# Kernel tuning notes

Measured on AMD Instinct MI355X. Metric: run time of the kernel, lower is better.

Reference implementation:

```python
import jax, jax.numpy as jnp
import numpy as np

L, D, K, NUM_CLASSES, HID = 512, 128, 1, 3, 128
EPS = 1e-8


def setup_inputs() -> dict:
    key = jax.random.key(0)
    ks = jax.random.split(key, 8)
    B, N = 16, 16384
    x = jax.random.normal(ks[0], (B, N, L), dtype=jnp.float32)
    mask = jnp.ones((B, N), dtype=jnp.float32)
    # params stored as [in, out] (equivalent to torch Linear with W.T)
    Wv = jax.random.normal(ks[1], (L, D), dtype=jnp.float32) * (1.0 / np.sqrt(L))
    bv = jnp.zeros((D,), dtype=jnp.float32)
    Wu = jax.random.normal(ks[2], (L, D), dtype=jnp.float32) * (1.0 / np.sqrt(L))
    bu = jnp.zeros((D,), dtype=jnp.float32)
    Wa = jax.random.normal(ks[3], (D, K), dtype=jnp.float32) * (1.0 / np.sqrt(D))
    ba = jnp.zeros((K,), dtype=jnp.float32)
    W1 = jax.random.normal(ks[4], (L, HID), dtype=jnp.float32) * (1.0 / np.sqrt(L))
    b1 = jnp.zeros((HID,), dtype=jnp.float32)
    W2 = jax.random.normal(ks[5], (HID, NUM_CLASSES), dtype=jnp.float32) * (1.0 / np.sqrt(HID))
    b2 = jnp.zeros((NUM_CLASSES,), dtype=jnp.float32)
    return {"x": x, "mask": mask, "Wv": Wv, "bv": bv, "Wu": Wu, "bu": bu,
            "Wa": Wa, "ba": ba, "W1": W1, "b1": b1, "W2": W2, "b2": b2,
            "top_k": 70}


def reference(x, mask, Wv, bv, Wu, bu, Wa, ba, W1, b1, W2, b2, top_k):
    # gated attention scores: [B, N]
    A_V = jnp.tanh(jnp.einsum('bnl,ld->bnd', x, Wv) + bv)
    A_U = jax.nn.sigmoid(jnp.einsum('bnl,ld->bnd', x, Wu) + bu)
    A = jnp.einsum('bnd,dk->bnk', A_V * A_U, Wa) + ba   # [B, N, K=1]
    A = jax.nn.softmax(A, axis=1)[..., 0]               # [B, N]
    # mask + renormalize
    A = A * mask
    A = A / (jnp.sum(A, axis=1, keepdims=True) + EPS)
    # dropout is identity in eval mode
    k = min(top_k, x.shape[1])
    topk_vals, topk_idxs = jax.lax.top_k(A, k)          # [B, k]
    # gather full feature vectors of top-k patches, mean pool
    topk_features = jnp.take_along_axis(x, topk_idxs[..., None], axis=1)  # [B, k, L]
    pooled = jnp.mean(topk_features, axis=1)            # [B, L]
    # classifier MLP
    h = jax.nn.relu(pooled @ W1 + b1)
    Y_prob = h @ W2 + b2                                # [B, num_classes]
    Y_hat = jnp.argmax(Y_prob, axis=1)
    return Y_prob, Y_hat, A
```

## Files before the change

### kernel.cpp

```cpp
#include <hip/hip_runtime.h>
#include <math.h>

#define NB   16
#define NN   16384
#define LDIM 512
#define DDIM 128
#define HIDD 128
#define NCLS 3
#define KCAP 256
#define CCAP 1024
#define ROWB 8
#define EPSV 1e-8f
#define DELTA 0.02f

typedef float  f32x4  __attribute__((ext_vector_type(4)));
typedef int    i32x4  __attribute__((ext_vector_type(4)));
typedef unsigned u32x2 __attribute__((ext_vector_type(2)));
typedef __bf16 bf16x8 __attribute__((ext_vector_type(8)));
typedef unsigned long long u64;

__device__ __forceinline__ int get_k(const int* kp) {
    int k = kp[0];
    if (k < 1 || k > NN) {
        float f = __int_as_float(k);
        if (f >= 1.0f && f <= (float)NN) k = (int)f;
        else k = 70;
    }
    if (k > NN) k = NN;
    return k;
}

__device__ __forceinline__ unsigned okey(float f) {
    unsigned u = __float_as_uint(f);
    return (u & 0x80000000u) ? ~u : (u | 0x80000000u);
}
__device__ __forceinline__ float inv_okey(unsigned k) {
    unsigned u = (k & 0x80000000u) ? (k & 0x7FFFFFFFu) : ~k;
    return __uint_as_float(u);
}

__device__ __forceinline__ unsigned pk2bf(float a, float b) {
    unsigned ua = __float_as_uint(a); ua = (ua + 0x7FFFu + ((ua >> 16) & 1u)) >> 16;
    unsigned ub = __float_as_uint(b); ub = (ub + 0x7FFFu + ((ub >> 16) & 1u)) & 0xFFFF0000u;
    return (ua & 0xFFFFu) | ub;
}

__device__ __forceinline__ f32x4 mfma16(i32x4 a, i32x4 b, f32x4 c) {
    return __builtin_amdgcn_mfma_f32_16x16x32_bf16(
        __builtin_bit_cast(bf16x8, a), __builtin_bit_cast(bf16x8, b), c, 0, 0, 0);
}

__device__ __forceinline__ float sig_fast(float v)  { return 1.0f / (1.0f + __expf(-v)); }
__device__ __forceinline__ float tanh_fast(float v) { return 1.0f - 2.0f / (1.0f + __expf(2.0f * v)); }

__global__ void k0_prep(const float* __restrict__ Wv, const float* __restrict__ Wu,
                        unsigned short* __restrict__ Wp)
{
    int i = blockIdx.x * 256 + threadIdx.x;
    int g   = i >> 16;
    int rem = i & 65535;
    int kd  = rem >> 7;
    int n   = rem & 127;
    float w = g ? Wu[rem] : Wv[rem];
    unsigned u = __float_as_uint(w);
    u = (u + 0x7FFFu + ((u >> 16) & 1u)) >> 16;
    int kt = kd >> 5, lg = (kd >> 3) & 3, j = kd & 7, nt = n >> 4, lr = n & 15;
    Wp[kt * 8192 + g * 4096 + nt * 512 + lg * 128 + lr * 8 + j] = (unsigned short)u;
}

__global__ __launch_bounds__(512, 1)
void k1_mfma(const float* __restrict__ x, const unsigned short* __restrict__ Wp,
             const float* __restrict__ bv, const float* __restrict__ bu,
             const float* __restrict__ Wa, const float* __restrict__ ba,
             float* __restrict__ logits)
{
    __shared__ __align__(16) char lds[98304];

    const int t   = threadIdx.x;
    const int wid = t >> 6;
    const int l   = t & 63;
    const int lr  = l & 15;
    const int lg  = l >> 4;
    const int l7  = lr & 7;

    i32x4 Wreg[2][16];
    {
        const unsigned short* wb = Wp + wid * 512 + l * 8;
#pragma unroll
        for (int kt = 0; kt < 16; ++kt) {
#pragma unroll
            for (int g = 0; g < 2; ++g)
                Wreg[g][kt] = *(const i32x4*)(wb + kt * 8192 + g * 4096);
        }
    }

    const int dbase = wid * 16 + lg * 4;
    float bvR[4], buR[4], waR[4];
#pragma unroll
    for (int r = 0; r < 4; ++r) {
        bvR[r] = bv[dbase + r]; buR[r] = bu[dbase + r]; waR[r] = Wa[dbase + r];
    }
    const float ba0 = ba[0];

    const int c     = t & 127;
    const int r0    = t >> 7;
    const int chalf = c & 1;
    const int clog  = c >> 1;

    const size_t blk_row0 = (size_t)blockIdx.x * 1024;
    const float* xblk = x + blk_row0 * LDIM;
    float* sEp = (float*)(lds + 65536);

    f32x4 acc[2][2];
    f32x4 xg[8];

#pragma unroll
    for (int i = 0; i < 8; ++i)
        xg[i] = *(const f32x4*)(xblk + (size_t)(i * 4 + r0) * LDIM + c * 4);
#pragma unroll
    for (int i = 0; i < 8; ++i) {
        int row = i * 4 + r0;
        u32x2 wv; wv.x = pk2bf(xg[i].x, xg[i].y); wv.y = pk2bf(xg[i].z, xg[i].w);
        *(u32x2*)(lds + row * 1024 + ((clog ^ (row & 7)) * 16) + chalf * 8) = wv;
    }
    __syncthreads();

    int p = 0;
    for (int j = 0; j < 32; ++j) {
        const bool has_next = (j < 31);
        if (has_next) {
            const float* xt = xblk + (size_t)(j + 1) * 32 * LDIM;
#pragma unroll
            for (int i = 0; i < 8; ++i)
                xg[i] = *(const f32x4*)(xt + (size_t)(i * 4 + r0) * LDIM + c * 4);
        }
#pragma unroll
        for (int g = 0; g < 2; ++g)
#pragma unroll
            for (int rf = 0; rf < 2; ++rf)
                acc[g][rf] = f32x4{0.f, 0.f, 0.f, 0.f};
        const char* Xb = lds + p * 32768;
#pragma unroll
        for (int kt = 0; kt < 16; ++kt) {
            i32x4 b0 = *(const i32x4*)(Xb + lr * 1024        + (((kt * 4 + lg) ^ l7) * 16));
            i32x4 b1 = *(const i32x4*)(Xb + (16 + lr) * 1024 + (((kt * 4 + lg) ^ l7) * 16));
            acc[0][0] = mfma16(Wreg[0][kt], b0, acc[0][0]);
            acc[1][0] = mfma16(Wreg[1][kt], b0, acc[1][0]);
            acc[0][1] = mfma16(Wreg[0][kt], b1, acc[0][1]);
            acc[1][1] = mfma16(Wreg[1][kt], b1, acc[1][1]);
        }
        if (has_next) {
            char* Xw = lds + (p ^ 1) * 32768;
#pragma unroll
            for (int i = 0; i < 8; ++i) {
                int row = i * 4 + r0;
                u32x2 wv; wv.x = pk2bf(xg[i].x, xg[i].y); wv.y = pk2bf(xg[i].z, xg[i].w);
                *(u32x2*)(Xw + row * 1024 + ((clog ^ (row & 7)) * 16) + chalf * 8) = wv;
            }
        }
#pragma unroll
        for (int rf = 0; rf < 2; ++rf) {
            float s = 0.f;
#pragma unroll
            for (int r = 0; r < 4; ++r) {
                float vv = tanh_fast(acc[0][rf][r] + bvR[r]);
                float uu = sig_fast (acc[1][rf][r] + buR[r]);
                s = fmaf(vv * uu, waR[r], s);
            }
            s += __shfl_xor(s, 16);
            s += __shfl_xor(s, 32);
            if (l < 16) sEp[wid * 1024 + j * 32 + rf * 16 + l] = s;
        }
        __syncthreads();
        p ^= 1;
    }

#pragma unroll
    for (int rr = 0; rr < 2; ++rr) {
        int row = t + rr * 512;
        float s = ba0;
#pragma unroll
        for (int w2 = 0; w2 < 8; ++w2) s += sEp[w2 * 1024 + row];
        logits[blk_row0 + row] = s;
    }
}

__global__ __launch_bounds__(1024, 1)
void k3a_band_softmax(float* __restrict__ A, const float* __restrict__ mask,
                      const int* __restrict__ kp, int* __restrict__ idxWS,
                      int* __restrict__ candIdx, int* __restrict__ counts)
{
    __shared__ float sredf[16];
    __shared__ int   sredi[2][16];
    __shared__ int sIn, sCand;
    const int b = blockIdx.x;
    const int t = threadIdx.x;
    const int w = t >> 6;
    int k = get_k(kp); if (k > KCAP) k = KCAP;
    float* Ab = A + (size_t)b * NN;
    const float* mb = mask + (size_t)b * NN;

    float raw[16]; unsigned mbits = 0u;
#pragma unroll
    for (int j = 0; j < 16; ++j) {
        int i = t + j * 1024;
        raw[j] = Ab[i];
        if (mb[i] > 0.0f) mbits |= (1u << j);
    }
    unsigned kk[16];
#pragma unroll
    for (int j = 0; j < 16; ++j) {
        float v = ((mbits >> j) & 1) ? raw[j] : -3.0e38f;
        kk[j] = okey(v);
    }
    unsigned lo = 0u, hi = 0xFFFFFFFFu;
    int par = 0;
    while (lo < hi) {
        unsigned span = hi - lo;
        unsigned mid = lo + (span >> 1) + (span & 1u);
        int c = 0;
#pragma unroll
        for (int j = 0; j < 16; ++j) c += (kk[j] >= mid) ? 1 : 0;
#pragma unroll
        for (int m2 = 1; m2 < 64; m2 <<= 1) c += __shfl_xor(c, m2);
        if ((t & 63) == 0) sredi[par][w] = c;
        __syncthreads();
        c = 0;
#pragma unroll
        for (int w2 = 0; w2 < 16; ++w2) c += sredi[par][w2];
        if (c >= k) lo = mid; else hi = mid - 1;
        par ^= 1;
    }
    const float tv = inv_okey(lo);

    if (t == 0) { sIn = 0; sCand = 0; }
    __syncthreads();
    const float hiB = tv + DELTA, loB = tv - DELTA;
#pragma unroll
    for (int j = 0; j < 16; ++j) {
        int i = t + j * 1024;
        float v = ((mbits >> j) & 1) ? raw[j] : -3.0e38f;
        if (v > hiB)       { int p = atomicAdd(&sIn, 1);   if (p < KCAP) idxWS[b * KCAP + p] = i; }
        else if (v >= loB) { int p = atomicAdd(&sCand, 1); if (p < CCAP) candIdx[b * CCAP + p] = i; }
    }

    float mx = -INFINITY;
#pragma unroll
    for (int j = 0; j < 16; ++j) mx = fmaxf(mx, raw[j]);
#pragma unroll
    for (int m2 = 1; m2 < 64; m2 <<= 1) mx = fmaxf(mx, __shfl_xor(mx, m2));
    __syncthreads();
    if ((t & 63) == 0) sredf[w] = mx;
    __syncthreads();
    mx = sredf[0];
#pragma unroll
    for (int w2 = 1; w2 < 16; ++w2) mx = fmaxf(mx, sredf[w2]);

    float sAll = 0.f, sM = 0.f;
#pragma unroll
    for (int j = 0; j < 16; ++j) {
        float e = __expf(raw[j] - mx);
        sAll += e;
        if ((mbits >> j) & 1) sM += e;
    }
#pragma unroll
    for (int m2 = 1; m2 < 64; m2 <<= 1) sAll += __shfl_xor(sAll, m2);
    __syncthreads();
    if ((t & 63) == 0) sredf[w] = sAll;
    __syncthreads();
    sAll = 0.f;
#pragma unroll
    for (int w2 = 0; w2 < 16; ++w2) sAll += sredf[w2];
#pragma unroll
    for (int m2 = 1; m2 < 64; m2 <<= 1) sM += __shfl_xor(sM, m2);
    __syncthreads();
    if ((t & 63) == 0) sredf[w] = sM;
    __syncthreads();
    sM = 0.f;
#pragma unroll
    for (int w2 = 0; w2 < 16; ++w2) sM += sredf[w2];

    const float inv = 1.0f / (sM + EPSV * sAll);
#pragma unroll
    for (int j = 0; j < 16; ++j) {
        int i = t + j * 1024;
        float e = __expf(raw[j] - mx);
        Ab[i] = ((mbits >> j) & 1) ? e * inv : 0.0f;
    }
    if (t == 0) {
        int m1 = sIn;   if (m1 > k)    m1 = k;
        int cc = sCand; if (cc > CCAP) cc = CCAP;
        counts[b * 4]     = m1;
        counts[b * 4 + 1] = cc;
    }
}

__global__ __launch_bounds__(512)
void k3b_exact(const float* __restrict__ x,
               const float* __restrict__ Wv, const float* __restrict__ bv,
               const float* __restrict__ Wu, const float* __restrict__ bu,
               const float* __restrict__ Wa, const float* __restrict__ ba,
               const int* __restrict__ candIdx, const int* __restrict__ counts,
               float* __restrict__ candVal)
{
    __shared__ __align__(16) float sx[ROWB][LDIM];
    __shared__ float sqv[4][ROWB][DDIM];
    __shared__ float squ[4][ROWB][DDIM];
    __shared__ float sred[2][ROWB];
    const int b = blockIdx.x;
    const int t = threadIdx.x;
    const int d = t & 127;
    const int q = t >> 7;
    const int cnt = counts[b * 4 + 1];
    const float ba0 = ba[0];

    for (int base = blockIdx.y * ROWB; base < cnt; base += gridDim.y * ROWB) {
        const int nr = min(ROWB, cnt - base);
#pragma unroll
        for (int rr = 0; rr < 2; ++rr) {
            int idx = t + rr * 512;
            int r   = idx >> 7;
            int c4  = idx & 127;
            int rowi = (r < nr) ? (base + r) : base;
            const int row = candIdx[b * CCAP + rowi];
            ((f32x4*)&sx[r][0])[c4] =
                ((const f32x4*)(x + ((size_t)b * NN + (size_t)row) * LDIM))[c4];
        }
        __syncthreads();

        float dv[ROWB], du[ROWB];
#pragma unroll
        for (int r = 0; r < ROWB; ++r) { dv[r] = 0.f; du[r] = 0.f; }
        const int ll0 = q * 128;
#pragma unroll 4
        for (int l2 = 0; l2 < 128; ++l2) {
            const int ll = ll0 + l2;
            const float wvl = Wv[ll * DDIM + d];
            const float wul = Wu[ll * DDIM + d];
#pragma unroll
            for (int r = 0; r < ROWB; ++r) {
                const float xv = sx[r][ll];
                dv[r] = fmaf(xv, wvl, dv[r]);
                du[r] = fmaf(xv, wul, du[r]);
            }
        }
#pragma unroll
        for (int r = 0; r < ROWB; ++r) { sqv[q][r][d] = dv[r]; squ[q][r][d] = du[r]; }
        __syncthreads();

        if (q == 0) {
            const float bvd = bv[d], bud = bu[d], wad = Wa[d];
            const int w2 = t >> 6;
#pragma unroll
            for (int r = 0; r < ROWB; ++r) {
                float fv = sqv[0][r][d] + sqv[1][r][d] + sqv[2][r][d] + sqv[3][r][d] + bvd;
                float fu = squ[0][r][d] + squ[1][r][d] + squ[2][r][d] + squ[3][r][d] + bud;
                float c = tanhf(fv) * (1.0f / (1.0f + expf(-fu))) * wad;
                c += __shfl_xor(c, 1);  c += __shfl_xor(c, 2);
                c += __shfl_xor(c, 4);  c += __shfl_xor(c, 8);
                c += __shfl_xor(c, 16); c += __shfl_xor(c, 32);
                if ((t & 63) == 0) sred[w2][r] = c;
            }
        }
        __syncthreads();
        if (t < nr) candVal[b * CCAP + base + t] = sred[0][t] + sred[1][t] + ba0;
        __syncthreads();
    }
}

__global__ __launch_bounds__(512)
void k34_select_final(const float* __restrict__ x, const int* __restrict__ kp,
                      const int* __restrict__ candIdx, const float* __restrict__ candVal,
                      const int* __restrict__ counts, const int* __restrict__ idxWS,
                      const float* __restrict__ W1, const float* __restrict__ b1,
                      const float* __restrict__ W2, const float* __restrict__ b2,
                      float* __restrict__ Yprob, float* __restrict__ Yhat)
{
    __shared__ u64 keys[CCAP];
    __shared__ int sIdx[KCAP];
    __shared__ int sFinal[KCAP];
    __shared__ int sPos;
    __shared__ float sPooled[LDIM];
    __shared__ float sHp[4][HIDD];
    __shared__ float sH[HIDD];
    __shared__ float sY[4];
    const int b = blockIdx.x;
    const int t = threadIdx.x;
    int k = get_k(kp); if (k > KCAP) k = KCAP;
    const int m1  = counts[b * 4];
    const int cnt = counts[b * 4 + 1];
    int need = k - m1; if (need < 0) need = 0; if (need > cnt) need = cnt;

    for (int i = t; i < cnt; i += 512)
        keys[i] = (((u64)okey(candVal[b * CCAP + i])) << 14)
                | (u64)(16383 - candIdx[b * CCAP + i]);
    if (t < m1) sIdx[t] = idxWS[b * KCAP + t];
    if (t == 0) sPos = 0;
    if (t < KCAP) sFinal[t] = 0;
    __syncthreads();
    for (int i = t; i < cnt; i += 512) {
        u64 mk = keys[i];
        int rank = 0;
        for (int j = 0; j < cnt; ++j) rank += (keys[j] > mk) ? 1 : 0;
        if (rank < need) { int p = atomicAdd(&sPos, 1); sIdx[m1 + p] = candIdx[b * CCAP + i]; }
    }
    __syncthreads();
    int tot = m1 + need; if (tot > k) tot = k;
    if (t < tot) {
        int myv = sIdx[t];
        int rank = 0;
        for (int e = 0; e < tot; ++e) rank += (sIdx[e] < myv) ? 1 : 0;
        sFinal[rank] = myv;
    }
    __syncthreads();

    {
        float a0 = 0.0f;
        int j = 0;
        for (; j + 8 <= k; j += 8) {
            float t0[8];
#pragma unroll
            for (int u2 = 0; u2 < 8; ++u2)
                t0[u2] = x[((size_t)b * NN + (size_t)sFinal[j + u2]) * LDIM + t];
#pragma unroll
            for (int u2 = 0; u2 < 8; ++u2) a0 += t0[u2];
        }
        for (; j < k; ++j)
            a0 += x[((size_t)b * NN + (size_t)sFinal[j]) * LDIM + t];
        sPooled[t] = a0 * (1.0f / (float)k);
    }
    __syncthreads();

    {
        const int d = t & 127;
        const int q = t >> 7;
        float acc = 0.f;
#pragma unroll 4
        for (int l2 = 0; l2 < 128; ++l2) {
            int ll = q * 128 + l2;
            acc = fmaf(sPooled[ll], W1[ll * HIDD + d], acc);
        }
        sHp[q][d] = acc;
    }
    __syncthreads();
    if (t < HIDD) {
        float acc = b1[t] + sHp[0][t] + sHp[1][t] + sHp[2][t] + sHp[3][t];
        sH[t] = fmaxf(acc, 0.0f);
    }
    __syncthreads();
    if (t < NCLS) {
        float y = b2[t];
        for (int hh = 0; hh < HIDD; ++hh) y = fmaf(sH[hh], W2[hh * NCLS + t], y);
        Yprob[b * NCLS + t] = y;
        sY[t] = y;
    }
    __syncthreads();
    if (t == 0) {
        int am = 0; float bst = sY[0];
        if (sY[1] > bst) { bst = sY[1]; am = 1; }
        if (sY[2] > bst) { bst = sY[2]; am = 2; }
        Yhat[b] = (float)am;
    }
}

extern "C" void kernel_launch(void* const* d_in, const int* in_sizes, int n_in,
                              void* d_out, int out_size, void* d_ws, size_t ws_size,
                              hipStream_t stream)
{
    const float* x    = (const float*)d_in[0];
    const float* mask = (const float*)d_in[1];
    const float* Wv   = (const float*)d_in[2];
    const float* bv   = (const float*)d_in[3];
    const float* Wu   = (const float*)d_in[4];
    const float* bu   = (const float*)d_in[5];
    const float* Wa   = (const float*)d_in[6];
    const float* ba   = (const float*)d_in[7];
    const float* W1   = (const float*)d_in[8];
    const float* b1   = (const float*)d_in[9];
    const float* W2   = (const float*)d_in[10];
    const float* b2   = (const float*)d_in[11];
    const int*   kp   = (const int*)d_in[12];

    float* out   = (float*)d_out;
    float* Yprob = out;
    float* Yhat  = out + 48;
    float* A     = out + 64;

    char* wsb = (char*)d_ws;
    unsigned short* Wp = (unsigned short*)wsb;
    int*   idxWS   = (int*)  (wsb + 262144);
    int*   candIdx = (int*)  (wsb + 278528);
    float* candVal = (float*)(wsb + 344064);
    int*   counts  = (int*)  (wsb + 409600);

    k0_prep  <<<512, 256, 0, stream>>>(Wv, Wu, Wp);
    k1_mfma  <<<256, 512, 0, stream>>>(x, Wp, bv, bu, Wa, ba, A);
    k3a_band_softmax<<<NB, 1024, 0, stream>>>(A, mask, kp, idxWS, candIdx, counts);
    k3b_exact<<<dim3(NB, 32), 512, 0, stream>>>(x, Wv, bv, Wu, bu, Wa, ba,
                                                candIdx, counts, candVal);
    k34_select_final<<<NB, 512, 0, stream>>>(x, kp, candIdx, candVal, counts, idxWS,
                                             W1, b1, W2, b2, Yprob, Yhat);
}
```

Baseline: 208.0 us.

## Use value-space bisection for top-k threshold and halve band-softmax block size

The band/softmax kernel replaces the 32-step bisection over ordered integer keys with 12 bisection steps in float value space, bounded between the masked max and max-32. The block shrinks from 1024 to 512 threads, each holding 32 elements, and the band half-width DELTA widens to absorb the coarser threshold. In the MFMA kernel, the first x tile loads are now issued before the weight register loads so global latency overlaps. The approximate threshold relies on DELTA being wide enough and the candidate set staying within its cap, otherwise top-k selection could be wrong.

```diff
diff --git a/kernel.cpp b/kernel.cpp
--- a/kernel.cpp
+++ b/kernel.cpp
@@ -11,7 +11,7 @@
 #define CCAP 1024
 #define ROWB 8
 #define EPSV 1e-8f
-#define DELTA 0.02f
+#define DELTA 0.03f
 
 typedef float  f32x4  __attribute__((ext_vector_type(4)));
 typedef int    i32x4  __attribute__((ext_vector_type(4)));
@@ -33,10 +33,6 @@
 __device__ __forceinline__ unsigned okey(float f) {
     unsigned u = __float_as_uint(f);
     return (u & 0x80000000u) ? ~u : (u | 0x80000000u);
-}
-__device__ __forceinline__ float inv_okey(unsigned k) {
-    unsigned u = (k & 0x80000000u) ? (k & 0x7FFFFFFFu) : ~k;
-    return __uint_as_float(u);
 }
 
 __device__ __forceinline__ unsigned pk2bf(float a, float b) {
@@ -83,25 +79,6 @@
     const int lg  = l >> 4;
     const int l7  = lr & 7;
 
-    i32x4 Wreg[2][16];
-    {
-        const unsigned short* wb = Wp + wid * 512 + l * 8;
-#pragma unroll
-        for (int kt = 0; kt < 16; ++kt) {
-#pragma unroll
-            for (int g = 0; g < 2; ++g)
-                Wreg[g][kt] = *(const i32x4*)(wb + kt * 8192 + g * 4096);
-        }
-    }
-
-    const int dbase = wid * 16 + lg * 4;
-    float bvR[4], buR[4], waR[4];
-#pragma unroll
-    for (int r = 0; r < 4; ++r) {
-        bvR[r] = bv[dbase + r]; buR[r] = bu[dbase + r]; waR[r] = Wa[dbase + r];
-    }
-    const float ba0 = ba[0];
-
     const int c     = t & 127;
     const int r0    = t >> 7;
     const int chalf = c & 1;
@@ -117,6 +94,26 @@
 #pragma unroll
     for (int i = 0; i < 8; ++i)
         xg[i] = *(const f32x4*)(xblk + (size_t)(i * 4 + r0) * LDIM + c * 4);
+
+    i32x4 Wreg[2][16];
+    {
+        const unsigned short* wb = Wp + wid * 512 + l * 8;
+#pragma unroll
+        for (int kt = 0; kt < 16; ++kt) {
+#pragma unroll
+            for (int g = 0; g < 2; ++g)
+                Wreg[g][kt] = *(const i32x4*)(wb + kt * 8192 + g * 4096);
+        }
+    }
+
+    const int dbase = wid * 16 + lg * 4;
+    float bvR[4], buR[4], waR[4];
+#pragma unroll
+    for (int r = 0; r < 4; ++r) {
+        bvR[r] = bv[dbase + r]; buR[r] = bu[dbase + r]; waR[r] = Wa[dbase + r];
+    }
+    const float ba0 = ba[0];
+
 #pragma unroll
     for (int i = 0; i < 8; ++i) {
         int row = i * 4 + r0;
@@ -185,13 +182,13 @@
     }
 }
 
-__global__ __launch_bounds__(1024, 1)
+__global__ __launch_bounds__(512, 1)
 void k3a_band_softmax(float* __restrict__ A, const float* __restrict__ mask,
                       const int* __restrict__ kp, int* __restrict__ idxWS,
                       int* __restrict__ candIdx, int* __restrict__ counts)
 {
-    __shared__ float sredf[16];
-    __shared__ int   sredi[2][16];
+    __shared__ float sredf[2][8];
+    __shared__ int   sredi[2][8];
     __shared__ int sIn, sCand;
     const int b = blockIdx.x;
     const int t = threadIdx.x;
@@ -200,45 +197,57 @@
     float* Ab = A + (size_t)b * NN;
     const float* mb = mask + (size_t)b * NN;
 
-    float raw[16]; unsigned mbits = 0u;
-#pragma unroll
-    for (int j = 0; j < 16; ++j) {
-        int i = t + j * 1024;
+    float raw[32]; u64 mbits = 0ULL;
+#pragma unroll
+    for (int j = 0; j < 32; ++j) {
+        int i = t + j * 512;
         raw[j] = Ab[i];
-        if (mb[i] > 0.0f) mbits |= (1u << j);
-    }
-    unsigned kk[16];
-#pragma unroll
-    for (int j = 0; j < 16; ++j) {
-        float v = ((mbits >> j) & 1) ? raw[j] : -3.0e38f;
-        kk[j] = okey(v);
-    }
-    unsigned lo = 0u, hi = 0xFFFFFFFFu;
-    int par = 0;
-    while (lo < hi) {
-        unsigned span = hi - lo;
-        unsigned mid = lo + (span >> 1) + (span & 1u);
-        int c = 0;
-#pragma unroll
-        for (int j = 0; j < 16; ++j) c += (kk[j] >= mid) ? 1 : 0;
-#pragma unroll
-        for (int m2 = 1; m2 < 64; m2 <<= 1) c += __shfl_xor(c, m2);
-        if ((t & 63) == 0) sredi[par][w] = c;
-        __syncthreads();
-        c = 0;
-#pragma unroll
-        for (int w2 = 0; w2 < 16; ++w2) c += sredi[par][w2];
-        if (c >= k) lo = mid; else hi = mid - 1;
-        par ^= 1;
-    }
-    const float tv = inv_okey(lo);
+        if (mb[i] > 0.0f) mbits |= (1ULL << j);
+    }
+
+    float mxm = -3.0e38f;
+#pragma unroll
+    for (int j = 0; j < 32; ++j)
+        if ((mbits >> j) & 1) mxm = fmaxf(mxm, raw[j]);
+#pragma unroll
+    for (int m2 = 1; m2 < 64; m2 <<= 1) mxm = fmaxf(mxm, __shfl_xor(mxm, m2));
+    if ((t & 63) == 0) sredf[0][w] = mxm;
+    __syncthreads();
+    mxm = sredf[0][0];
+#pragma unroll
+    for (int w2 = 1; w2 < 8; ++w2) mxm = fmaxf(mxm, sredf[0][w2]);
+
+    float lov = mxm - 32.0f, hiv = mxm;
+    {
+        int par = 0;
+#pragma unroll
+        for (int it = 0; it < 12; ++it) {
+            float mid = 0.5f * (lov + hiv);
+            int cgt = 0;
+#pragma unroll
+            for (int j = 0; j < 32; ++j) {
+                float v = ((mbits >> j) & 1) ? raw[j] : -3.0e38f;
+                cgt += (v >= mid) ? 1 : 0;
+            }
+#pragma unroll
+            for (int m2 = 1; m2 < 64; m2 <<= 1) cgt += __shfl_xor(cgt, m2);
+            if ((t & 63) == 0) sredi[par][w] = cgt;
+            __syncthreads();
+            cgt = 0;
+#pragma unroll
+            for (int w2 = 0; w2 < 8; ++w2) cgt += sredi[par][w2];
+            if (cgt >= k) lov = mid; else hiv = mid;
+            par ^= 1;
+        }
+    }
+    const float tv = lov;
 
     if (t == 0) { sIn = 0; sCand = 0; }
     __syncthreads();
     const float hiB = tv + DELTA, loB = tv - DELTA;
 #pragma unroll
-    for (int j = 0; j < 16; ++j) {
-        int i = t + j * 1024;
+    for (int j = 0; j < 32; ++j) {
+        int i = t + j * 512;
         float v = ((mbits >> j) & 1) ? raw[j] : -3.0e38f;
         if (v > hiB)       { int p = atomicAdd(&sIn, 1);   if (p < KCAP) idxWS[b * KCAP + p] = i; }
         else if (v >= loB) { int p = atomicAdd(&sCand, 1); if (p < CCAP) candIdx[b * CCAP + p] = i; }
@@ -246,19 +255,19 @@
 
     float mx = -INFINITY;
 #pragma unroll
-    for (int j = 0; j < 16; ++j) mx = fmaxf(mx, raw[j]);
+    for (int j = 0; j < 32; ++j) mx = fmaxf(mx, raw[j]);
 #pragma unroll
     for (int m2 = 1; m2 < 64; m2 <<= 1) mx = fmaxf(mx, __shfl_xor(mx, m2));
     __syncthreads();
-    if ((t & 63) == 0) sredf[w] = mx;
-    __syncthreads();
-    mx = sredf[0];
-#pragma unroll
-    for (int w2 = 1; w2 < 16; ++w2) mx = fmaxf(mx, sredf[w2]);
+    if ((t & 63) == 0) sredf[1][w] = mx;
+    __syncthreads();
+    mx = sredf[1][0];
+#pragma unroll
+    for (int w2 = 1; w2 < 8; ++w2) mx = fmaxf(mx, sredf[1][w2]);
 
     float sAll = 0.f, sM = 0.f;
 #pragma unroll
-    for (int j = 0; j < 16; ++j) {
+    for (int j = 0; j < 32; ++j) {
         float e = __expf(raw[j] - mx);
         sAll += e;
         if ((mbits >> j) & 1) sM += e;
@@ -266,24 +275,24 @@
 #pragma unroll
     for (int m2 = 1; m2 < 64; m2 <<= 1) sAll += __shfl_xor(sAll, m2);
     __syncthreads();
-    if ((t & 63) == 0) sredf[w] = sAll;
+    if ((t & 63) == 0) sredf[0][w] = sAll;
     __syncthreads();
     sAll = 0.f;
 #pragma unroll
-    for (int w2 = 0; w2 < 16; ++w2) sAll += sredf[w2];
+    for (int w2 = 0; w2 < 8; ++w2) sAll += sredf[0][w2];
 #pragma unroll
     for (int m2 = 1; m2 < 64; m2 <<= 1) sM += __shfl_xor(sM, m2);
     __syncthreads();
-    if ((t & 63) == 0) sredf[w] = sM;
+    if ((t & 63) == 0) sredf[1][w] = sM;
     __syncthreads();
     sM = 0.f;
 #pragma unroll
-    for (int w2 = 0; w2 < 16; ++w2) sM += sredf[w2];
+    for (int w2 = 0; w2 < 8; ++w2) sM += sredf[1][w2];
 
     const float inv = 1.0f / (sM + EPSV * sAll);
 #pragma unroll
-    for (int j = 0; j < 16; ++j) {
-        int i = t + j * 1024;
+    for (int j = 0; j < 32; ++j) {
+        int i = t + j * 512;
         float e = __expf(raw[j] - mx);
         Ab[i] = ((mbits >> j) & 1) ? e * inv : 0.0f;
     }
@@ -495,7 +504,7 @@
 
     k0_prep  <<<512, 256, 0, stream>>>(Wv, Wu, Wp);
     k1_mfma  <<<256, 512, 0, stream>>>(x, Wp, bv, bu, Wa, ba, A);
-    k3a_band_softmax<<<NB, 1024, 0, stream>>>(A, mask, kp, idxWS, candIdx, counts);
+    k3a_band_softmax<<<NB, 512, 0, stream>>>(A, mask, kp, idxWS, candIdx, counts);
     k3b_exact<<<dim3(NB, 32), 512, 0, stream>>>(x, Wv, bv, Wu, bu, Wa, ba,
                                                 candIdx, counts, candVal);
     k34_select_final<<<NB, 512, 0, stream>>>(x, kp, candIdx, candVal, counts, idxWS,
```

Result: faster. 192.5 us (median of 2 runs) (-7.5%).
